# Kernel tuning notes

Measured on AMD Instinct MI355X. Metric: run time of the kernel, lower is better.

The kernel has to match this reference:

```python
import jax, jax.numpy as jnp
import numpy as np

N = 2_000_000
FUN, TAU, ALPHA, LOSS_WEIGHT = 'log', 1.0, 1.0, 1.0


def setup_inputs() -> dict:
    key = jax.random.key(0)
    k1, k2, k3 = jax.random.split(key, 3)
    pred = jax.random.uniform(k1, (N, 5), dtype=jnp.float32)
    target = jax.random.uniform(k2, (N, 5), dtype=jnp.float32)
    weight = jax.random.uniform(k3, (N,), dtype=jnp.float32)
    return {"pred": pred, "target": target, "weight": weight}


def _xyrs(xywhr):
    # [N,5] -> xy [N,2], R [N,2,2], S [N,2,2] (diag(wh/2))
    xy = xywhr[:, :2]
    wh = xywhr[:, 2:4]
    r = xywhr[:, 4]
    c, s = jnp.cos(r), jnp.sin(r)
    R = jnp.stack([c, -s, s, c], axis=-1).reshape(-1, 2, 2)
    S = 0.5 * wh[:, :, None] * jnp.eye(2, dtype=xywhr.dtype)  # diag_embed
    return xy, R, S


def _sqrt_trace_2x2sym(M):
    # trace of matrix sqrt of symmetric PSD 2x2: sqrt(tr(M) + 2*sqrt(det(M)))
    a, b, d = M[:, 0, 0], M[:, 0, 1], M[:, 1, 1]
    det = jnp.clip(a * d - b * b, 0.0)
    return jnp.sqrt(jnp.clip(a + d + 2.0 * jnp.sqrt(det), 0.0))


def reference(pred, target, weight):
    xy_p, R_p, S_p = _xyrs(pred)
    xy_t, R_t, S_t = _xyrs(target)

    dxy = xy_p - xy_t
    xy_distance = jnp.sum(dxy * dxy, axis=-1)

    Rp_T = jnp.swapaxes(R_p, -1, -2)
    Rt_T = jnp.swapaxes(R_t, -1, -2)
    Sigma_p_sqrt = R_p @ S_p @ Rp_T
    Sigma_p = R_p @ (S_p * S_p) @ Rp_T
    Sigma_t = R_t @ (S_t * S_t) @ Rt_T

    whr_distance = Sigma_p[:, 0, 0] + Sigma_p[:, 1, 1]
    whr_distance = whr_distance + Sigma_t[:, 0, 0] + Sigma_t[:, 1, 1]
    cross = Sigma_p_sqrt @ Sigma_t @ Sigma_p_sqrt
    whr_distance = whr_distance - 2.0 * _sqrt_trace_2x2sym(cross)

    distance = jnp.sqrt(jnp.clip(xy_distance + ALPHA * whr_distance, 0.0))
    scale = jnp.sqrt(jnp.sqrt(jnp.prod(pred[:, 2:4] * target[:, 2:4], axis=-1)))
    distance = distance / scale

    if FUN == 'log':
        distance = jnp.log1p(distance)
    elif FUN == 'sqrt':
        distance = jnp.sqrt(distance)

    if TAU >= 1.0:
        loss = 1.0 - 1.0 / (TAU + distance)
    else:
        loss = distance

    # weighted_loss wrapper: elementwise weight then mean reduction
    loss = jnp.mean(loss * weight)
    return loss * LOSS_WEIGHT
```

## Files before the change

kernel.cpp:

```cpp
#include <hip/hip_runtime.h>


#define NBLK 1024

__device__ __forceinline__ float gwd_row(const float* __restrict__ p,
                                         const float* __restrict__ t)
{
    const float px = p[0], py = p[1], pw = p[2], ph = p[3], pr = p[4];
    const float tx = t[0], ty = t[1], tw = t[2], th = t[3], tr = t[4];

    const float dx = px - tx;
    const float dy = py - ty;
    const float xy_dist = dx * dx + dy * dy;

    const float a2p = 0.25f * pw * pw;
    const float b2p = 0.25f * ph * ph;
    const float a2t = 0.25f * tw * tw;
    const float b2t = 0.25f * th * th;

    float whr = (a2p + b2p) + (a2t + b2t);

    float cp, sp, ct, st;
    __sincosf(pr, &sp, &cp);
    __sincosf(tr, &st, &ct);

    const float Sp00 = cp * cp * a2p + sp * sp * b2p;
    const float Sp01 = cp * sp * (a2p - b2p);
    const float Sp11 = sp * sp * a2p + cp * cp * b2p;
    const float St00 = ct * ct * a2t + st * st * b2t;
    const float St01 = ct * st * (a2t - b2t);
    const float St11 = st * st * a2t + ct * ct * b2t;

    const float tr_cross  = Sp00 * St00 + 2.0f * Sp01 * St01 + Sp11 * St11;
    const float det_cross = (a2p * b2p) * (a2t * b2t);

    const float sq = fmaxf(tr_cross + 2.0f * __builtin_amdgcn_sqrtf(det_cross), 0.0f);
    whr = whr - 2.0f * __builtin_amdgcn_sqrtf(sq);

    float d = __builtin_amdgcn_sqrtf(fmaxf(xy_dist + whr, 0.0f));

    const float prod = (pw * tw) * (ph * th);
    d *= __builtin_amdgcn_rsqf(__builtin_amdgcn_sqrtf(prod));

    d = 0.69314718056f * __builtin_amdgcn_logf(1.0f + d);

    return 1.0f - __builtin_amdgcn_rcpf(1.0f + d);
}

__global__ __launch_bounds__(256) void gwd_partial(
    const float* __restrict__ pred,
    const float* __restrict__ target,
    const float* __restrict__ weight,
    float* __restrict__ ws,
    int n)
{
    const int tid = threadIdx.x;
    const int ngroups = n >> 2;
    float acc = 0.0f;

    for (int g = blockIdx.x * 256 + tid; g < ngroups; g += NBLK * 256) {
        const float4* p4 = (const float4*)pred   + (size_t)g * 5;
        const float4* t4 = (const float4*)target + (size_t)g * 5;

        float4 P[5], T[5];
        #pragma unroll
        for (int j = 0; j < 5; ++j) P[j] = p4[j];
        #pragma unroll
        for (int j = 0; j < 5; ++j) T[j] = t4[j];
        const float4 w4 = ((const float4*)weight)[g];

        float pbuf[20], tbuf[20];
        #pragma unroll
        for (int j = 0; j < 5; ++j) { *(float4*)(pbuf + 4 * j) = P[j];
                                      *(float4*)(tbuf + 4 * j) = T[j]; }
        const float w[4] = { w4.x, w4.y, w4.z, w4.w };
        #pragma unroll
        for (int j = 0; j < 4; ++j)
            acc += gwd_row(&pbuf[j * 5], &tbuf[j * 5]) * w[j];
    }

    #pragma unroll
    for (int off = 32; off > 0; off >>= 1)
        acc += __shfl_down(acc, off, 64);

    __shared__ float wave_sums[4];
    const int lane = tid & 63;
    const int wid  = tid >> 6;
    if (lane == 0) wave_sums[wid] = acc;
    __syncthreads();

    if (tid == 0)
        ws[blockIdx.x] = (wave_sums[0] + wave_sums[1]) + (wave_sums[2] + wave_sums[3]);
}

__global__ __launch_bounds__(256) void gwd_final(
    const float* __restrict__ ws,
    const float* __restrict__ pred,
    const float* __restrict__ target,
    const float* __restrict__ weight,
    float* __restrict__ out,
    int n)
{
    const int tid = threadIdx.x;
    float acc = 0.0f;

    #pragma unroll
    for (int j = 0; j < NBLK / 256; ++j)
        acc += ws[j * 256 + tid];

    const int tail0 = n & ~3;
    if (tid < (n - tail0)) {
        const int r = tail0 + tid;
        float pb[5], tb[5];
        #pragma unroll
        for (int k = 0; k < 5; ++k) {
            pb[k] = pred  [(size_t)r * 5 + k];
            tb[k] = target[(size_t)r * 5 + k];
        }
        acc += gwd_row(pb, tb) * weight[r];
    }

    #pragma unroll
    for (int off = 32; off > 0; off >>= 1)
        acc += __shfl_down(acc, off, 64);

    __shared__ float wave_sums[4];
    const int lane = tid & 63;
    const int wid  = tid >> 6;
    if (lane == 0) wave_sums[wid] = acc;
    __syncthreads();

    if (tid == 0) {
        const float s = (wave_sums[0] + wave_sums[1]) + (wave_sums[2] + wave_sums[3]);
        out[0] = s * (1.0f / (float)n);
    }
}

extern "C" void kernel_launch(void* const* d_in, const int* in_sizes, int n_in,
                              void* d_out, int out_size, void* d_ws, size_t ws_size,
                              hipStream_t stream) {
    const float* pred   = (const float*)d_in[0];
    const float* target = (const float*)d_in[1];
    const float* weight = (const float*)d_in[2];
    float* out = (float*)d_out;
    float* ws  = (float*)d_ws;

    const int n = in_sizes[2];

    gwd_partial<<<NBLK, 256, 0, stream>>>(pred, target, weight, ws, n);
    gwd_final<<<1, 256, 0, stream>>>(ws, pred, target, weight, out, n);
}
```

Before: 107.3 us.

## Fuse partial and final reductions into one kernel via last-block atomic ticket

Replaces the two-kernel reduction with one kernel. Each block publishes its partial sum, then takes an agent-scope acquire-release atomic ticket, and the last block to arrive does the final sum, handles the tail rows and writes the mean. The ticket is reset each call with a hipMemsetAsync, which adds a memset operation to the stream in place of the second kernel launch. This targets launch and inter-kernel gap overhead but relies on correct memory ordering between blocks.

```diff
diff --git a/kernel.cpp b/kernel.cpp
--- a/kernel.cpp
+++ b/kernel.cpp
@@ -47,6 +47,106 @@
     return 1.0f - __builtin_amdgcn_rcpf(1.0f + d);
 }
 
+__device__ __forceinline__ float gwd_accum(const float* __restrict__ pred,
+                                           const float* __restrict__ target,
+                                           const float* __restrict__ weight,
+                                           int n)
+{
+    const int tid = threadIdx.x;
+    const int ngroups = n >> 2;
+    float acc = 0.0f;
+
+    for (int g = blockIdx.x * 256 + tid; g < ngroups; g += NBLK * 256) {
+        const float4* p4 = (const float4*)pred   + (size_t)g * 5;
+        const float4* t4 = (const float4*)target + (size_t)g * 5;
+
+        float4 P[5], T[5];
+        #pragma unroll
+        for (int j = 0; j < 5; ++j) P[j] = p4[j];
+        #pragma unroll
+        for (int j = 0; j < 5; ++j) T[j] = t4[j];
+        const float4 w4 = ((const float4*)weight)[g];
+
+        float pbuf[20], tbuf[20];
+        #pragma unroll
+        for (int j = 0; j < 5; ++j) { *(float4*)(pbuf + 4 * j) = P[j];
+                                      *(float4*)(tbuf + 4 * j) = T[j]; }
+        const float w[4] = { w4.x, w4.y, w4.z, w4.w };
+        #pragma unroll
+        for (int j = 0; j < 4; ++j)
+            acc += gwd_row(&pbuf[j * 5], &tbuf[j * 5]) * w[j];
+    }
+    return acc;
+}
+
+
+__global__ __launch_bounds__(256) void gwd_fused(
+    const float* __restrict__ pred,
+    const float* __restrict__ target,
+    const float* __restrict__ weight,
+    float* __restrict__ ws,
+    unsigned int* __restrict__ ticket,
+    float* __restrict__ out,
+    int n)
+{
+    const int tid  = threadIdx.x;
+    const int lane = tid & 63;
+    const int wid  = tid >> 6;
+    __shared__ float wave_sums[4];
+    __shared__ bool am_last;
+
+    float acc = gwd_accum(pred, target, weight, n);
+
+    #pragma unroll
+    for (int off = 32; off > 0; off >>= 1)
+        acc += __shfl_down(acc, off, 64);
+
+    if (lane == 0) wave_sums[wid] = acc;
+    __syncthreads();
+
+    if (tid == 0) {
+        const float s = (wave_sums[0] + wave_sums[1]) + (wave_sums[2] + wave_sums[3]);
+        __hip_atomic_store(&ws[blockIdx.x], s, __ATOMIC_RELAXED,
+                           __HIP_MEMORY_SCOPE_AGENT);
+        const unsigned int old = __hip_atomic_fetch_add(
+            ticket, 1u, __ATOMIC_ACQ_REL, __HIP_MEMORY_SCOPE_AGENT);
+        am_last = (old == NBLK - 1);
+    }
+    __syncthreads();
+
+    if (!am_last) return;
+
+    float a2 = 0.0f;
+    #pragma unroll
+    for (int j = 0; j < NBLK / 256; ++j)
+        a2 += __hip_atomic_load(&ws[j * 256 + tid], __ATOMIC_RELAXED,
+                                __HIP_MEMORY_SCOPE_AGENT);
+
+    const int tail0 = n & ~3;
+    if (tid < (n - tail0)) {
+        const int r = tail0 + tid;
+        float pb[5], tb[5];
+        #pragma unroll
+        for (int k = 0; k < 5; ++k) {
+            pb[k] = pred  [(size_t)r * 5 + k];
+            tb[k] = target[(size_t)r * 5 + k];
+        }
+        a2 += gwd_row(pb, tb) * weight[r];
+    }
+
+    #pragma unroll
+    for (int off = 32; off > 0; off >>= 1)
+        a2 += __shfl_down(a2, off, 64);
+
+    if (lane == 0) wave_sums[wid] = a2;
+    __syncthreads();
+    if (tid == 0) {
+        const float s = (wave_sums[0] + wave_sums[1]) + (wave_sums[2] + wave_sums[3]);
+        out[0] = s * (1.0f / (float)n);
+    }
+}
+
+
 __global__ __launch_bounds__(256) void gwd_partial(
     const float* __restrict__ pred,
     const float* __restrict__ target,
@@ -55,29 +155,7 @@
     int n)
 {
     const int tid = threadIdx.x;
-    const int ngroups = n >> 2;
-    float acc = 0.0f;
-
-    for (int g = blockIdx.x * 256 + tid; g < ngroups; g += NBLK * 256) {
-        const float4* p4 = (const float4*)pred   + (size_t)g * 5;
-        const float4* t4 = (const float4*)target + (size_t)g * 5;
-
-        float4 P[5], T[5];
-        #pragma unroll
-        for (int j = 0; j < 5; ++j) P[j] = p4[j];
-        #pragma unroll
-        for (int j = 0; j < 5; ++j) T[j] = t4[j];
-        const float4 w4 = ((const float4*)weight)[g];
-
-        float pbuf[20], tbuf[20];
-        #pragma unroll
-        for (int j = 0; j < 5; ++j) { *(float4*)(pbuf + 4 * j) = P[j];
-                                      *(float4*)(tbuf + 4 * j) = T[j]; }
-        const float w[4] = { w4.x, w4.y, w4.z, w4.w };
-        #pragma unroll
-        for (int j = 0; j < 4; ++j)
-            acc += gwd_row(&pbuf[j * 5], &tbuf[j * 5]) * w[j];
-    }
+    float acc = gwd_accum(pred, target, weight, n);
 
     #pragma unroll
     for (int off = 32; off > 0; off >>= 1)
@@ -144,9 +222,17 @@
     const float* weight = (const float*)d_in[2];
     float* out = (float*)d_out;
     float* ws  = (float*)d_ws;
+    unsigned int* ticket = (unsigned int*)(ws + NBLK);
 
     const int n = in_sizes[2];
 
-    gwd_partial<<<NBLK, 256, 0, stream>>>(pred, target, weight, ws, n);
-    gwd_final<<<1, 256, 0, stream>>>(ws, pred, target, weight, out, n);
-}
+    hipError_t e = hipMemsetAsync(ticket, 0, sizeof(unsigned int), stream);
+    if (e == hipSuccess) {
+        gwd_fused<<<NBLK, 256, 0, stream>>>(pred, target, weight, ws, ticket,
+                                            out, n);
+    } else {
+        (void)hipGetLastError();
+        gwd_partial<<<NBLK, 256, 0, stream>>>(pred, target, weight, ws, n);
+        gwd_final<<<1, 256, 0, stream>>>(ws, pred, target, weight, out, n);
+    }
+}
```

After: 149.5 us. 1.39x slower.
